# Kernel tuning notes

Measured on AMD Instinct MI355X. Metric: run time of the kernel, lower is better.

The kernel has to match this reference:

```python
import jax, jax.numpy as jnp
import numpy as np

TEMPERATURE = 0.5
N, D = 8192, 256
N_CLASSES = 100

def setup_inputs() -> dict:
    key = jax.random.key(0)
    k0, k1, k2 = jax.random.split(key, 3)
    out0 = jax.random.normal(k0, (N, D), dtype=jnp.float32)
    out1 = jax.random.normal(k1, (N, D), dtype=jnp.float32)
    labels = jax.random.randint(k2, (N,), 0, N_CLASSES, dtype=jnp.int64)
    return {"out0": out0, "out1": out1, "labels": labels}

def _l2_normalize(x, eps=1e-12):
    # matches torch.nn.functional.normalize(dim=1)
    norm = jnp.sqrt(jnp.sum(x * x, axis=1, keepdims=True))
    return x / jnp.maximum(norm, eps)

def reference(out0, out1, labels):
    a = _l2_normalize(out0)
    b = _l2_normalize(out1)
    logits = jnp.matmul(a, b.T) / TEMPERATURE            # [N, N]
    logits_exp = jnp.exp(logits)
    positive_mask = (labels[:, None] == labels[None, :]) # [N, N] bool
    pos_sum = jnp.sum(logits_exp * positive_mask, axis=1)
    all_sum = jnp.sum(logits_exp, axis=1)
    loss = -jnp.mean(jnp.log(pos_sum / all_sum))
    return loss
```

## Files before the change

### kernel.cpp

```cpp
#include <hip/hip_runtime.h>
#include <hip/hip_bf16.h>
#include <math.h>

#define N_ROWS 8192
#define D_DIM  256
#define BM 128
#define BN 64
#define JSPLIT 8
#define JRANGE (N_ROWS / JSPLIT)
#define NT (JRANGE / BN)

typedef __attribute__((ext_vector_type(4))) float f32x4;
typedef __attribute__((ext_vector_type(4))) int   i32x4;
typedef __attribute__((ext_vector_type(8))) int   i32x8;

#define CAST_SCALE 1.6986388f
#define SCALE_ONE 127

__device__ __forceinline__ float fast_exp2(float x) {
#if __has_builtin(__builtin_amdgcn_exp2f)
    return __builtin_amdgcn_exp2f(x);
#else
    return exp2f(x);
#endif
}

__global__ void norm_cast_kernel(const float* __restrict__ out0,
                                 const float* __restrict__ out1,
                                 unsigned char* __restrict__ a_f8,
                                 unsigned char* __restrict__ b_f8,
                                 float* __restrict__ zero_me,
                                 float* __restrict__ out) {
    int gtid = blockIdx.x * blockDim.x + threadIdx.x;
    if (gtid < 2 * N_ROWS) zero_me[gtid] = 0.0f;
    if (gtid == 0) out[0] = 0.0f;

    int wave = gtid >> 6;
    int lane = threadIdx.x & 63;
    const float* src    = (wave < N_ROWS) ? out0 : out1;
    unsigned char* dst  = (wave < N_ROWS) ? a_f8 : b_f8;
    int row = (wave < N_ROWS) ? wave : wave - N_ROWS;

    float4 v = *reinterpret_cast<const float4*>(src + (size_t)row * D_DIM + lane * 4);
    float ss = v.x * v.x + v.y * v.y + v.z * v.z + v.w * v.w;
    #pragma unroll
    for (int off = 32; off; off >>= 1) ss += __shfl_xor(ss, off);
    float inv = CAST_SCALE / fmaxf(sqrtf(ss), 1e-12f);

    int packed = __builtin_amdgcn_cvt_pk_fp8_f32(v.x * inv, v.y * inv, 0, 0);
    packed     = __builtin_amdgcn_cvt_pk_fp8_f32(v.z * inv, v.w * inv, packed, 1);
    *reinterpret_cast<unsigned int*>(dst + (size_t)row * D_DIM + lane * 4) =
        (unsigned int)packed;
}

__global__ __launch_bounds__(256, 2)
void fused_flash_kernel(const unsigned char* __restrict__ A,
                        const unsigned char* __restrict__ B,
                        const int* __restrict__ labels,
                        float* __restrict__ pos_sum,
                        float* __restrict__ all_sum) {
    __shared__ unsigned char Bs[3][BN * D_DIM];

    const int tid    = threadIdx.x;
    const int lane   = tid & 63;
    const int wid    = tid >> 6;
    const int wr     = wid >> 1;
    const int wc     = wid & 1;
    const int lane16 = lane & 15;
    const int kgrp   = lane >> 4;

    const int jsplit = blockIdx.x & 7;
    const int rowt   = blockIdx.x >> 3;
    const int i0     = rowt * BM;
    const int jbase  = jsplit * JRANGE;

    i32x8 af[4][2];
    #pragma unroll
    for (int m = 0; m < 4; ++m) {
        const unsigned char* ap =
            A + (size_t)(i0 + wr * 64 + m * 16 + lane16) * D_DIM + kgrp * 32;
        #pragma unroll
        for (int h = 0; h < 2; ++h) {
            i32x4 lo = *reinterpret_cast<const i32x4*>(ap + h * 128);
            i32x4 hi = *reinterpret_cast<const i32x4*>(ap + h * 128 + 16);
            af[m][h] = __builtin_shufflevector(lo, hi, 0, 1, 2, 3, 4, 5, 6, 7);
        }
    }
    #pragma unroll
    for (int m = 0; m < 4; ++m)
        #pragma unroll
        for (int h = 0; h < 2; ++h)
            asm volatile("" : "+v"(af[m][h]));

    int labp[4];
    #pragma unroll
    for (int m = 0; m < 4; ++m) {
        int4 v = *reinterpret_cast<const int4*>(labels + i0 + wr * 64 + m * 16 + kgrp * 4);
        labp[m] = v.x | (v.y << 8) | (v.z << 16) | (v.w << 24);
        asm volatile("" : "+v"(labp[m]));
    }

    auto stage = [&](int buf, int t) {
        const int jrow0 = jbase + t * BN;
        #pragma unroll
        for (int cc = 0; cc < 4; ++cc) {
            int c  = wid * 4 + cc;
            int gr = jrow0 + c * 4 + kgrp;
            const unsigned char* src =
                B + (size_t)gr * D_DIM + ((lane16 ^ (gr & 15)) << 4);
            __builtin_amdgcn_global_load_lds(
                (const __attribute__((address_space(1))) void*)src,
                (__attribute__((address_space(3))) void*)(&Bs[buf][0] + c * 1024),
                16, 0, 0);
        }
    };

    float allp[4][4] = {};
    float posp[4][4] = {};

    stage(0, 0);
    stage(1, 1);
    asm volatile("s_waitcnt vmcnt(4)" ::: "memory");
    __builtin_amdgcn_sched_barrier(0);
    __builtin_amdgcn_s_barrier();
    __builtin_amdgcn_sched_barrier(0);

    int cur = 0;
    for (int t = 0; t < NT; ++t) {
        const int jc    = jbase + t * BN + wc * 32 + lane16;
        const int labc0 = labels[jc];
        const int labc1 = labels[jc + 16];

        i32x8 bv[2][2];
        #pragma unroll
        for (int n = 0; n < 2; ++n) {
            const int tr = wc * 32 + n * 16 + lane16;
            #pragma unroll
            for (int h = 0; h < 2; ++h) {
                int g0 = h * 8 + kgrp * 2;
                i32x4 lo = *reinterpret_cast<const i32x4*>(
                    &Bs[cur][0] + tr * 256 + ((g0 ^ lane16) << 4));
                i32x4 hi = *reinterpret_cast<const i32x4*>(
                    &Bs[cur][0] + tr * 256 + (((g0 + 1) ^ lane16) << 4));
                bv[n][h] = __builtin_shufflevector(lo, hi, 0, 1, 2, 3, 4, 5, 6, 7);
            }
        }

        f32x4 acc[4][2] = {};
        __builtin_amdgcn_s_setprio(1);
        #pragma unroll
        for (int h = 0; h < 2; ++h)
            #pragma unroll
            for (int m = 0; m < 4; ++m)
                #pragma unroll
                for (int n = 0; n < 2; ++n)
                    acc[m][n] = __builtin_amdgcn_mfma_scale_f32_16x16x128_f8f6f4(
                        af[m][h], bv[n][h], acc[m][n],
                        0, 0,
                        0, SCALE_ONE,
                        0, SCALE_ONE);
        __builtin_amdgcn_s_setprio(0);

        if (t + 2 < NT) stage((cur + 2) % 3, t + 2);

        if (t < NT - 1) {
            if (t + 2 < NT) asm volatile("s_waitcnt vmcnt(4)" ::: "memory");
            else            asm volatile("s_waitcnt vmcnt(0)" ::: "memory");
            __builtin_amdgcn_sched_barrier(0);
            __builtin_amdgcn_s_barrier();
            __builtin_amdgcn_sched_barrier(0);
        }

        #pragma unroll
        for (int m = 0; m < 4; ++m) {
            #pragma unroll
            for (int r = 0; r < 4; ++r) {
                float e0 = fast_exp2(acc[m][0][r]);
                float e1 = fast_exp2(acc[m][1][r]);
                allp[m][r] += e0 + e1;
                int lr = (labp[m] >> (r * 8)) & 0xFF;
                posp[m][r] += (lr == labc0 ? e0 : 0.0f) + (lr == labc1 ? e1 : 0.0f);
            }
        }

        cur = (cur + 1) % 3;
    }

    #pragma unroll
    for (int m = 0; m < 4; ++m) {
        #pragma unroll
        for (int r = 0; r < 4; ++r) {
            float a = allp[m][r], p = posp[m][r];
            #pragma unroll
            for (int off = 1; off < 16; off <<= 1) {
                a += __shfl_xor(a, off);
                p += __shfl_xor(p, off);
            }
            if (lane16 == 0) {
                int grow = i0 + wr * 64 + m * 16 + kgrp * 4 + r;
                atomicAdd(&all_sum[grow], a);
                atomicAdd(&pos_sum[grow], p);
            }
        }
    }
}

__global__ void loss_kernel(const float* __restrict__ pos_sum,
                            const float* __restrict__ all_sum,
                            float* __restrict__ out) {
    int gid = blockIdx.x * blockDim.x + threadIdx.x;
    float acc = 0.0f;
    for (int i = gid; i < N_ROWS; i += gridDim.x * blockDim.x)
        acc += logf(pos_sum[i] / all_sum[i]);
    #pragma unroll
    for (int off = 32; off; off >>= 1) acc += __shfl_xor(acc, off);
    __shared__ float red[8];
    int wv = threadIdx.x >> 6, lane = threadIdx.x & 63;
    if (lane == 0) red[wv] = acc;
    __syncthreads();
    if (threadIdx.x == 0) {
        float s = 0.0f;
        #pragma unroll
        for (int w = 0; w < 8; ++w) s += red[w];
        atomicAdd(out, -s / (float)N_ROWS);
    }
}

extern "C" void kernel_launch(void* const* d_in, const int* in_sizes, int n_in,
                              void* d_out, int out_size, void* d_ws, size_t ws_size,
                              hipStream_t stream) {
    const float* out0   = (const float*)d_in[0];
    const float* out1   = (const float*)d_in[1];
    const int*   labels = (const int*)d_in[2];
    float*       out    = (float*)d_out;

    unsigned char* a_f8 = (unsigned char*)d_ws;
    unsigned char* b_f8 = a_f8 + (size_t)N_ROWS * D_DIM;
    float* pos  = (float*)(b_f8 + (size_t)N_ROWS * D_DIM);
    float* alls = pos + N_ROWS;

    norm_cast_kernel<<<2 * N_ROWS / 4, 256, 0, stream>>>(out0, out1, a_f8, b_f8, pos, out);

    fused_flash_kernel<<<JSPLIT * (N_ROWS / BM), 256, 0, stream>>>(a_f8, b_f8, labels, pos, alls);

    loss_kernel<<<16, 512, 0, stream>>>(pos, alls, out);
}
```

Before: 42.12 us.

## Use 8 waves per block, each owning a 64x16 output subtile

Doubles the block to 512 threads with 8 waves arranged 2x4, so each wave computes 64 rows by 16 columns per tile instead of 64 by 32. Per-wave B fragment loads, MFMAs and exp work are halved, and each wave issues fewer staging loads. The aim is more waves in flight to hide the exp and LDS latency. In exchange each A fragment (held in registers) is now replicated across four waves instead of two, and the barrier synchronizes more waves.

```diff
diff --git a/kernel.cpp b/kernel.cpp
--- a/kernel.cpp
+++ b/kernel.cpp
@@ -53,7 +53,7 @@
         (unsigned int)packed;
 }
 
-__global__ __launch_bounds__(256, 2)
+__global__ __launch_bounds__(512, 2)
 void fused_flash_kernel(const unsigned char* __restrict__ A,
                         const unsigned char* __restrict__ B,
                         const int* __restrict__ labels,
@@ -64,8 +64,8 @@
     const int tid    = threadIdx.x;
     const int lane   = tid & 63;
     const int wid    = tid >> 6;
-    const int wr     = wid >> 1;
-    const int wc     = wid & 1;
+    const int wr     = wid >> 2;
+    const int wq     = wid & 3;
     const int lane16 = lane & 15;
     const int kgrp   = lane >> 4;
 
@@ -103,8 +103,8 @@
     auto stage = [&](int buf, int t) {
         const int jrow0 = jbase + t * BN;
         #pragma unroll
-        for (int cc = 0; cc < 4; ++cc) {
-            int c  = wid * 4 + cc;
+        for (int cc = 0; cc < 2; ++cc) {
+            int c  = wid * 2 + cc;
             int gr = jrow0 + c * 4 + kgrp;
             const unsigned char* src =
                 B + (size_t)gr * D_DIM + ((lane16 ^ (gr & 15)) << 4);
@@ -120,51 +120,44 @@
 
     stage(0, 0);
     stage(1, 1);
-    asm volatile("s_waitcnt vmcnt(4)" ::: "memory");
+    asm volatile("s_waitcnt vmcnt(2)" ::: "memory");
     __builtin_amdgcn_sched_barrier(0);
     __builtin_amdgcn_s_barrier();
     __builtin_amdgcn_sched_barrier(0);
 
     int cur = 0;
     for (int t = 0; t < NT; ++t) {
-        const int jc    = jbase + t * BN + wc * 32 + lane16;
-        const int labc0 = labels[jc];
-        const int labc1 = labels[jc + 16];
-
-        i32x8 bv[2][2];
-        #pragma unroll
-        for (int n = 0; n < 2; ++n) {
-            const int tr = wc * 32 + n * 16 + lane16;
-            #pragma unroll
-            for (int h = 0; h < 2; ++h) {
-                int g0 = h * 8 + kgrp * 2;
-                i32x4 lo = *reinterpret_cast<const i32x4*>(
-                    &Bs[cur][0] + tr * 256 + ((g0 ^ lane16) << 4));
-                i32x4 hi = *reinterpret_cast<const i32x4*>(
-                    &Bs[cur][0] + tr * 256 + (((g0 + 1) ^ lane16) << 4));
-                bv[n][h] = __builtin_shufflevector(lo, hi, 0, 1, 2, 3, 4, 5, 6, 7);
-            }
-        }
-
-        f32x4 acc[4][2] = {};
+        const int labc = labels[jbase + t * BN + wq * 16 + lane16];
+
+        const int tr = wq * 16 + lane16;
+        i32x8 bv[2];
+        #pragma unroll
+        for (int h = 0; h < 2; ++h) {
+            int g0 = h * 8 + kgrp * 2;
+            i32x4 lo = *reinterpret_cast<const i32x4*>(
+                &Bs[cur][0] + tr * 256 + ((g0 ^ lane16) << 4));
+            i32x4 hi = *reinterpret_cast<const i32x4*>(
+                &Bs[cur][0] + tr * 256 + (((g0 + 1) ^ lane16) << 4));
+            bv[h] = __builtin_shufflevector(lo, hi, 0, 1, 2, 3, 4, 5, 6, 7);
+        }
+
+        f32x4 acc[4] = {};
         __builtin_amdgcn_s_setprio(1);
         #pragma unroll
         for (int h = 0; h < 2; ++h)
             #pragma unroll
             for (int m = 0; m < 4; ++m)
-                #pragma unroll
-                for (int n = 0; n < 2; ++n)
-                    acc[m][n] = __builtin_amdgcn_mfma_scale_f32_16x16x128_f8f6f4(
-                        af[m][h], bv[n][h], acc[m][n],
-                        0, 0,
-                        0, SCALE_ONE,
-                        0, SCALE_ONE);
+                acc[m] = __builtin_amdgcn_mfma_scale_f32_16x16x128_f8f6f4(
+                    af[m][h], bv[h], acc[m],
+                    0, 0,
+                    0, SCALE_ONE,
+                    0, SCALE_ONE);
         __builtin_amdgcn_s_setprio(0);
 
         if (t + 2 < NT) stage((cur + 2) % 3, t + 2);
 
         if (t < NT - 1) {
-            if (t + 2 < NT) asm volatile("s_waitcnt vmcnt(4)" ::: "memory");
+            if (t + 2 < NT) asm volatile("s_waitcnt vmcnt(2)" ::: "memory");
             else            asm volatile("s_waitcnt vmcnt(0)" ::: "memory");
             __builtin_amdgcn_sched_barrier(0);
             __builtin_amdgcn_s_barrier();
@@ -175,11 +168,10 @@
         for (int m = 0; m < 4; ++m) {
             #pragma unroll
             for (int r = 0; r < 4; ++r) {
-                float e0 = fast_exp2(acc[m][0][r]);
-                float e1 = fast_exp2(acc[m][1][r]);
-                allp[m][r] += e0 + e1;
+                float e = fast_exp2(acc[m][r]);
+                allp[m][r] += e;
                 int lr = (labp[m] >> (r * 8)) & 0xFF;
-                posp[m][r] += (lr == labc0 ? e0 : 0.0f) + (lr == labc1 ? e1 : 0.0f);
+                posp[m][r] += (lr == labc) ? e : 0.0f;
             }
         }
 
@@ -241,7 +233,7 @@
 
     norm_cast_kernel<<<2 * N_ROWS / 4, 256, 0, stream>>>(out0, out1, a_f8, b_f8, pos, out);
 
-    fused_flash_kernel<<<JSPLIT * (N_ROWS / BM), 256, 0, stream>>>(a_f8, b_f8, labels, pos, alls);
+    fused_flash_kernel<<<JSPLIT * (N_ROWS / BM), 512, 0, stream>>>(a_f8, b_f8, labels, pos, alls);
 
     loss_kernel<<<16, 512, 0, stream>>>(pos, alls, out);
 }
```

Result: slower. 58.62 us (+39.2%).

## Software-pipeline exp epilogue of previous tile with MFMAs of current tile

Applied to the files above, without the earlier changes.

The main loop now keeps two sets of accumulators and is unrolled by two. While the MFMAs for tile t are issued, the exp2, label-mask and row-sum epilogue runs on the results of tile t-1, so transcendental and VALU work can overlap matrix-core work instead of following it. Each MFMA chain now starts from a zero vector instead of a zero-initialised accumulator array. The cost is about 32 more live accumulator VGPRs, which could raise register pressure, plus more code from the macro expansion.

```diff
diff --git a/kernel.cpp b/kernel.cpp
--- a/kernel.cpp
+++ b/kernel.cpp
@@ -53,6 +53,60 @@
         (unsigned int)packed;
 }
 
+
+#define BV_LOAD(BV)                                                            \
+    _Pragma("unroll")                                                          \
+    for (int n = 0; n < 2; ++n) {                                              \
+        const int tr = wc * 32 + n * 16 + lane16;                              \
+        _Pragma("unroll")                                                      \
+        for (int h = 0; h < 2; ++h) {                                          \
+            int g0 = h * 8 + kgrp * 2;                                         \
+            i32x4 lo = *reinterpret_cast<const i32x4*>(                        \
+                &Bs[cur][0] + tr * 256 + ((g0 ^ lane16) << 4));                \
+            i32x4 hi = *reinterpret_cast<const i32x4*>(                        \
+                &Bs[cur][0] + tr * 256 + (((g0 + 1) ^ lane16) << 4));          \
+            BV[n][h] = __builtin_shufflevector(lo, hi, 0, 1, 2, 3, 4, 5, 6, 7);\
+        }                                                                      \
+    }
+
+#define MFMA_BLOCK(ACC, BV)                                                    \
+    __builtin_amdgcn_s_setprio(1);                                             \
+    _Pragma("unroll")                                                          \
+    for (int m = 0; m < 4; ++m)                                                \
+        _Pragma("unroll")                                                      \
+        for (int n = 0; n < 2; ++n) {                                          \
+            ACC[m][n] = __builtin_amdgcn_mfma_scale_f32_16x16x128_f8f6f4(      \
+                af[m][0], BV[n][0], zero4, 0, 0, 0, SCALE_ONE, 0, SCALE_ONE);  \
+            ACC[m][n] = __builtin_amdgcn_mfma_scale_f32_16x16x128_f8f6f4(      \
+                af[m][1], BV[n][1], ACC[m][n], 0, 0, 0, SCALE_ONE, 0, SCALE_ONE);\
+        }                                                                      \
+    __builtin_amdgcn_s_setprio(0);
+
+#define EPILOGUE(ACC, LC0, LC1)                                                \
+    _Pragma("unroll")                                                          \
+    for (int m = 0; m < 4; ++m) {                                              \
+        _Pragma("unroll")                                                      \
+        for (int r = 0; r < 4; ++r) {                                          \
+            float e0 = fast_exp2(ACC[m][0][r]);                                \
+            float e1 = fast_exp2(ACC[m][1][r]);                                \
+            allp[m][r] += e0 + e1;                                             \
+            int lr = (labp[m] >> (r * 8)) & 0xFF;                              \
+            posp[m][r] += ((lr == (LC0)) ? e0 : 0.0f)                          \
+                        + ((lr == (LC1)) ? e1 : 0.0f);                         \
+        }                                                                      \
+    }
+
+#define SYNC_STEP(T)                                                           \
+    if ((T) + 2 < NT) stage((cur + 2) % 3, (T) + 2);                           \
+    if ((T) < NT - 1) {                                                        \
+        if ((T) + 2 < NT) asm volatile("s_waitcnt vmcnt(4)" ::: "memory");     \
+        else              asm volatile("s_waitcnt vmcnt(0)" ::: "memory");     \
+        __builtin_amdgcn_sched_barrier(0);                                     \
+        __builtin_amdgcn_s_barrier();                                          \
+        __builtin_amdgcn_sched_barrier(0);                                     \
+    }                                                                          \
+    cur = (cur + 1) % 3;
+
 __global__ __launch_bounds__(256, 2)
 void fused_flash_kernel(const unsigned char* __restrict__ A,
                         const unsigned char* __restrict__ B,
@@ -73,6 +127,8 @@
     const int rowt   = blockIdx.x >> 3;
     const int i0     = rowt * BM;
     const int jbase  = jsplit * JRANGE;
+
+    const f32x4 zero4 = {};
 
     i32x8 af[4][2];
     #pragma unroll
@@ -117,6 +173,8 @@
 
     float allp[4][4] = {};
     float posp[4][4] = {};
+    f32x4 accA[4][2], accB[4][2];
+    int lcA0 = 0, lcA1 = 0, lcB0 = 0, lcB1 = 0;
 
     stage(0, 0);
     stage(1, 1);
@@ -126,65 +184,41 @@
     __builtin_amdgcn_sched_barrier(0);
 
     int cur = 0;
-    for (int t = 0; t < NT; ++t) {
-        const int jc    = jbase + t * BN + wc * 32 + lane16;
-        const int labc0 = labels[jc];
-        const int labc1 = labels[jc + 16];
-
+
+    {
+        const int jc = jbase + 0 * BN + wc * 32 + lane16;
+        lcA0 = labels[jc];
+        lcA1 = labels[jc + 16];
         i32x8 bv[2][2];
-        #pragma unroll
-        for (int n = 0; n < 2; ++n) {
-            const int tr = wc * 32 + n * 16 + lane16;
-            #pragma unroll
-            for (int h = 0; h < 2; ++h) {
-                int g0 = h * 8 + kgrp * 2;
-                i32x4 lo = *reinterpret_cast<const i32x4*>(
-                    &Bs[cur][0] + tr * 256 + ((g0 ^ lane16) << 4));
-                i32x4 hi = *reinterpret_cast<const i32x4*>(
-                    &Bs[cur][0] + tr * 256 + (((g0 + 1) ^ lane16) << 4));
-                bv[n][h] = __builtin_shufflevector(lo, hi, 0, 1, 2, 3, 4, 5, 6, 7);
-            }
-        }
-
-        f32x4 acc[4][2] = {};
-        __builtin_amdgcn_s_setprio(1);
-        #pragma unroll
-        for (int h = 0; h < 2; ++h)
-            #pragma unroll
-            for (int m = 0; m < 4; ++m)
-                #pragma unroll
-                for (int n = 0; n < 2; ++n)
-                    acc[m][n] = __builtin_amdgcn_mfma_scale_f32_16x16x128_f8f6f4(
-                        af[m][h], bv[n][h], acc[m][n],
-                        0, 0,
-                        0, SCALE_ONE,
-                        0, SCALE_ONE);
-        __builtin_amdgcn_s_setprio(0);
-
-        if (t + 2 < NT) stage((cur + 2) % 3, t + 2);
-
-        if (t < NT - 1) {
-            if (t + 2 < NT) asm volatile("s_waitcnt vmcnt(4)" ::: "memory");
-            else            asm volatile("s_waitcnt vmcnt(0)" ::: "memory");
-            __builtin_amdgcn_sched_barrier(0);
-            __builtin_amdgcn_s_barrier();
-            __builtin_amdgcn_sched_barrier(0);
-        }
-
-        #pragma unroll
-        for (int m = 0; m < 4; ++m) {
-            #pragma unroll
-            for (int r = 0; r < 4; ++r) {
-                float e0 = fast_exp2(acc[m][0][r]);
-                float e1 = fast_exp2(acc[m][1][r]);
-                allp[m][r] += e0 + e1;
-                int lr = (labp[m] >> (r * 8)) & 0xFF;
-                posp[m][r] += (lr == labc0 ? e0 : 0.0f) + (lr == labc1 ? e1 : 0.0f);
-            }
-        }
-
-        cur = (cur + 1) % 3;
-    }
+        BV_LOAD(bv);
+        MFMA_BLOCK(accA, bv);
+        SYNC_STEP(0);
+    }
+
+    for (int tt = 1; tt < NT; tt += 2) {
+        {
+            const int jc = jbase + tt * BN + wc * 32 + lane16;
+            lcB0 = labels[jc];
+            lcB1 = labels[jc + 16];
+            i32x8 bv[2][2];
+            BV_LOAD(bv);
+            EPILOGUE(accA, lcA0, lcA1);
+            MFMA_BLOCK(accB, bv);
+            SYNC_STEP(tt);
+        }
+        if (tt + 1 < NT) {
+            const int t2 = tt + 1;
+            const int jc = jbase + t2 * BN + wc * 32 + lane16;
+            lcA0 = labels[jc];
+            lcA1 = labels[jc + 16];
+            i32x8 bv[2][2];
+            BV_LOAD(bv);
+            EPILOGUE(accB, lcB0, lcB1);
+            MFMA_BLOCK(accA, bv);
+            SYNC_STEP(t2);
+        }
+    }
+    EPILOGUE(accB, lcB0, lcB1);
 
     #pragma unroll
     for (int m = 0; m < 4; ++m) {
```

New measurement: 44.04 us. 1.05x slower.

## Quantize normalized embeddings to FP4 and use FP4 scaled MFMA

Applied to the files above, without the earlier changes.

Encodes the normalized rows into 4-bit e2m1 values with a custom encoder, which halves the packed row size, and switches the scaled MFMA to the FP4 format with an adjusted block scale. This halves global and LDS traffic for both operands and the number of staging loads, and the FP4 MFMA has higher throughput. The trade-off is much coarser quantization of the logits feeding exp, which risks accuracy beyond tolerance.

```diff
diff --git a/kernel.cpp b/kernel.cpp
--- a/kernel.cpp
+++ b/kernel.cpp
@@ -4,6 +4,7 @@
 
 #define N_ROWS 8192
 #define D_DIM  256
+#define ROWB   128
 #define BM 128
 #define BN 64
 #define JSPLIT 8
@@ -14,8 +15,8 @@
 typedef __attribute__((ext_vector_type(4))) int   i32x4;
 typedef __attribute__((ext_vector_type(8))) int   i32x8;
 
-#define CAST_SCALE 1.6986388f
-#define SCALE_ONE 127
+#define CAST_G    27.17835f
+#define SCALE_Q16 123
 
 __device__ __forceinline__ float fast_exp2(float x) {
 #if __has_builtin(__builtin_amdgcn_exp2f)
@@ -25,10 +26,18 @@
 #endif
 }
 
+__device__ __forceinline__ unsigned int enc_fp4(float x) {
+    float a = fabsf(x);
+    unsigned int s = (__float_as_uint(x) >> 31) << 3;
+    unsigned int c = (a > 0.25f) + (a > 0.75f) + (a > 1.25f) + (a > 1.75f)
+                   + (a > 2.5f)  + (a > 3.5f)  + (a > 5.0f);
+    return s | c;
+}
+
 __global__ void norm_cast_kernel(const float* __restrict__ out0,
                                  const float* __restrict__ out1,
-                                 unsigned char* __restrict__ a_f8,
-                                 unsigned char* __restrict__ b_f8,
+                                 unsigned char* __restrict__ a_f4,
+                                 unsigned char* __restrict__ b_f4,
                                  float* __restrict__ zero_me,
                                  float* __restrict__ out) {
     int gtid = blockIdx.x * blockDim.x + threadIdx.x;
@@ -38,19 +47,21 @@
     int wave = gtid >> 6;
     int lane = threadIdx.x & 63;
     const float* src    = (wave < N_ROWS) ? out0 : out1;
-    unsigned char* dst  = (wave < N_ROWS) ? a_f8 : b_f8;
+    unsigned char* dst  = (wave < N_ROWS) ? a_f4 : b_f4;
     int row = (wave < N_ROWS) ? wave : wave - N_ROWS;
 
     float4 v = *reinterpret_cast<const float4*>(src + (size_t)row * D_DIM + lane * 4);
     float ss = v.x * v.x + v.y * v.y + v.z * v.z + v.w * v.w;
     #pragma unroll
     for (int off = 32; off; off >>= 1) ss += __shfl_xor(ss, off);
-    float inv = CAST_SCALE / fmaxf(sqrtf(ss), 1e-12f);
-
-    int packed = __builtin_amdgcn_cvt_pk_fp8_f32(v.x * inv, v.y * inv, 0, 0);
-    packed     = __builtin_amdgcn_cvt_pk_fp8_f32(v.z * inv, v.w * inv, packed, 1);
-    *reinterpret_cast<unsigned int*>(dst + (size_t)row * D_DIM + lane * 4) =
-        (unsigned int)packed;
+    float inv = CAST_G / fmaxf(sqrtf(ss), 1e-12f);
+
+    unsigned int p = enc_fp4(v.x * inv)
+                   | (enc_fp4(v.y * inv) << 4)
+                   | (enc_fp4(v.z * inv) << 8)
+                   | (enc_fp4(v.w * inv) << 12);
+    *reinterpret_cast<unsigned short*>(dst + (size_t)row * ROWB + lane * 2) =
+        (unsigned short)p;
 }
 
 __global__ __launch_bounds__(256, 2)
@@ -59,7 +70,7 @@
                         const int* __restrict__ labels,
                         float* __restrict__ pos_sum,
                         float* __restrict__ all_sum) {
-    __shared__ unsigned char Bs[3][BN * D_DIM];
+    __shared__ unsigned char Bs[3][BN * ROWB];
 
     const int tid    = threadIdx.x;
     const int lane   = tid & 63;
@@ -74,17 +85,16 @@
     const int i0     = rowt * BM;
     const int jbase  = jsplit * JRANGE;
 
-    i32x8 af[4][2];
+    const i32x4 zeros = {0, 0, 0, 0};
+
+    i32x4 af[4][2];
     #pragma unroll
     for (int m = 0; m < 4; ++m) {
         const unsigned char* ap =
-            A + (size_t)(i0 + wr * 64 + m * 16 + lane16) * D_DIM + kgrp * 32;
-        #pragma unroll
-        for (int h = 0; h < 2; ++h) {
-            i32x4 lo = *reinterpret_cast<const i32x4*>(ap + h * 128);
-            i32x4 hi = *reinterpret_cast<const i32x4*>(ap + h * 128 + 16);
-            af[m][h] = __builtin_shufflevector(lo, hi, 0, 1, 2, 3, 4, 5, 6, 7);
-        }
+            A + (size_t)(i0 + wr * 64 + m * 16 + lane16) * ROWB + kgrp * 16;
+        #pragma unroll
+        for (int h = 0; h < 2; ++h)
+            af[m][h] = *reinterpret_cast<const i32x4*>(ap + h * 64);
     }
     #pragma unroll
     for (int m = 0; m < 4; ++m)
@@ -103,11 +113,11 @@
     auto stage = [&](int buf, int t) {
         const int jrow0 = jbase + t * BN;
         #pragma unroll
-        for (int cc = 0; cc < 4; ++cc) {
-            int c  = wid * 4 + cc;
-            int gr = jrow0 + c * 4 + kgrp;
+        for (int cc = 0; cc < 2; ++cc) {
+            int c  = wid * 2 + cc;
+            int gr = jrow0 + c * 8 + (lane >> 3);
             const unsigned char* src =
-                B + (size_t)gr * D_DIM + ((lane16 ^ (gr & 15)) << 4);
+                B + (size_t)gr * ROWB + (((lane & 7) ^ (gr & 7)) << 4);
             __builtin_amdgcn_global_load_lds(
                 (const __attribute__((address_space(1))) void*)src,
                 (__attribute__((address_space(3))) void*)(&Bs[buf][0] + c * 1024),
@@ -120,7 +130,7 @@
 
     stage(0, 0);
     stage(1, 1);
-    asm volatile("s_waitcnt vmcnt(4)" ::: "memory");
+    asm volatile("s_waitcnt vmcnt(2)" ::: "memory");
     __builtin_amdgcn_sched_barrier(0);
     __builtin_amdgcn_s_barrier();
     __builtin_amdgcn_sched_barrier(0);
@@ -131,18 +141,15 @@
         const int labc0 = labels[jc];
         const int labc1 = labels[jc + 16];
 
-        i32x8 bv[2][2];
+        i32x4 bv[2][2];
         #pragma unroll
         for (int n = 0; n < 2; ++n) {
             const int tr = wc * 32 + n * 16 + lane16;
             #pragma unroll
             for (int h = 0; h < 2; ++h) {
-                int g0 = h * 8 + kgrp * 2;
-                i32x4 lo = *reinterpret_cast<const i32x4*>(
-                    &Bs[cur][0] + tr * 256 + ((g0 ^ lane16) << 4));
-                i32x4 hi = *reinterpret_cast<const i32x4*>(
-                    &Bs[cur][0] + tr * 256 + (((g0 + 1) ^ lane16) << 4));
-                bv[n][h] = __builtin_shufflevector(lo, hi, 0, 1, 2, 3, 4, 5, 6, 7);
+                int g = h * 4 + kgrp;
+                bv[n][h] = *reinterpret_cast<const i32x4*>(
+                    &Bs[cur][0] + tr * ROWB + ((g ^ (tr & 7)) << 4));
             }
         }
 
@@ -151,20 +158,24 @@
         #pragma unroll
         for (int h = 0; h < 2; ++h)
             #pragma unroll
-            for (int m = 0; m < 4; ++m)
+            for (int m = 0; m < 4; ++m) {
+                i32x8 a8 = __builtin_shufflevector(af[m][h], zeros, 0,1,2,3,4,5,6,7);
                 #pragma unroll
-                for (int n = 0; n < 2; ++n)
+                for (int n = 0; n < 2; ++n) {
+                    i32x8 b8 = __builtin_shufflevector(bv[n][h], zeros, 0,1,2,3,4,5,6,7);
                     acc[m][n] = __builtin_amdgcn_mfma_scale_f32_16x16x128_f8f6f4(
-                        af[m][h], bv[n][h], acc[m][n],
-                        0, 0,
-                        0, SCALE_ONE,
-                        0, SCALE_ONE);
+                        a8, b8, acc[m][n],
+                        4, 4,
+                        0, SCALE_Q16,
+                        0, SCALE_Q16);
+                }
+            }
         __builtin_amdgcn_s_setprio(0);
 
         if (t + 2 < NT) stage((cur + 2) % 3, t + 2);
 
         if (t < NT - 1) {
-            if (t + 2 < NT) asm volatile("s_waitcnt vmcnt(4)" ::: "memory");
+            if (t + 2 < NT) asm volatile("s_waitcnt vmcnt(2)" ::: "memory");
             else            asm volatile("s_waitcnt vmcnt(0)" ::: "memory");
             __builtin_amdgcn_sched_barrier(0);
             __builtin_amdgcn_s_barrier();
@@ -234,14 +245,14 @@
     const int*   labels = (const int*)d_in[2];
     float*       out    = (float*)d_out;
 
-    unsigned char* a_f8 = (unsigned char*)d_ws;
-    unsigned char* b_f8 = a_f8 + (size_t)N_ROWS * D_DIM;
-    float* pos  = (float*)(b_f8 + (size_t)N_ROWS * D_DIM);
+    unsigned char* a_f4 = (unsigned char*)d_ws;
+    unsigned char* b_f4 = a_f4 + (size_t)N_ROWS * ROWB;
+    float* pos  = (float*)(b_f4 + (size_t)N_ROWS * ROWB);
     float* alls = pos + N_ROWS;
 
-    norm_cast_kernel<<<2 * N_ROWS / 4, 256, 0, stream>>>(out0, out1, a_f8, b_f8, pos, out);
-
-    fused_flash_kernel<<<JSPLIT * (N_ROWS / BM), 256, 0, stream>>>(a_f8, b_f8, labels, pos, alls);
+    norm_cast_kernel<<<2 * N_ROWS / 4, 256, 0, stream>>>(out0, out1, a_f4, b_f4, pos, out);
+
+    fused_flash_kernel<<<JSPLIT * (N_ROWS / BM), 256, 0, stream>>>(a_f4, b_f4, labels, pos, alls);
 
     loss_kernel<<<16, 512, 0, stream>>>(pos, alls, out);
 }
```

Result: faster. 36.59 us (-13.1%).
